# Performance work log

Hardware: AMD Instinct MI355X
Metric: run time of the kernel (lower is better)

Reference implementation:

```python
import jax, jax.numpy as jnp
import numpy as np

RATIO = 0.2
MIX_ALPHA = 0.5
TEMPERATURE = 0.1
EPS = 1e-12  # F.normalize eps


def setup_inputs() -> dict:
    key = jax.random.key(0)
    z = jax.random.normal(key, (16384, 256), dtype=jnp.float32)
    return {"z": z}


def reference(z):
    B = z.shape[0]
    n_hard = max(1, int(B * RATIO))

    # L2-normalize rows (F.normalize with eps clamp)
    norm = jnp.maximum(jnp.linalg.norm(z, axis=-1, keepdims=True), EPS)
    z_norm = z / norm

    # [B, B] cosine similarity, diagonal excluded
    sim = z_norm @ z_norm.T
    diag = jnp.eye(B, dtype=bool)
    sim = jnp.where(diag, -jnp.inf, sim)
    logits = sim / TEMPERATURE  # softmax(logits) == sim_probs

    # Batched sampling: replaces the per-sample Python loop with one fused pass
    key = jax.random.key(42)
    k_src, k_tgt, k_alpha = jax.random.split(key, 3)
    src_idx = jax.random.randint(k_src, (n_hard,), 0, B)  # torch.randint
    # categorical over logits rows == multinomial over softmax probs
    tgt_idx = jax.random.categorical(k_tgt, logits[src_idx], axis=-1)
    alpha = jax.random.uniform(k_alpha, (n_hard, 1), dtype=z.dtype) * MIX_ALPHA

    hard_negs = alpha * z[src_idx] + (1.0 - alpha) * z[tgt_idx]  # [n_hard, D]
    return hard_negs
```

## Files before the change

### kernel.cpp

```cpp
#include <hip/hip_runtime.h>
#include <stdint.h>
#include <math.h>

#define BN 16384
#define DK 256
#define NH 3276
#define NJB 52
#define NCB 128
#define NTILE (NJB * NCB)

typedef __attribute__((ext_vector_type(8))) short short8;
typedef __attribute__((ext_vector_type(4))) short short4v;
typedef __attribute__((ext_vector_type(4))) float f32x4;

__host__ __device__ __forceinline__ void tf2x32(uint32_t k0, uint32_t k1,
                                                uint32_t c0, uint32_t c1,
                                                uint32_t& o0, uint32_t& o1) {
  uint32_t ks2 = 0x1BD11BDAu ^ k0 ^ k1;
  uint32_t x0 = c0 + k0, x1 = c1 + k1;
#define RR(d) { x0 += x1; x1 = (x1 << d) | (x1 >> (32 - d)); x1 ^= x0; }
  RR(13) RR(15) RR(26) RR(6)   x0 += k1;  x1 += ks2 + 1u;
  RR(17) RR(29) RR(16) RR(24)  x0 += ks2; x1 += k0  + 2u;
  RR(13) RR(15) RR(26) RR(6)   x0 += k0;  x1 += k1  + 3u;
  RR(17) RR(29) RR(16) RR(24)  x0 += k1;  x1 += ks2 + 4u;
  RR(13) RR(15) RR(26) RR(6)   x0 += ks2; x1 += k0  + 5u;
#undef RR
  o0 = x0; o1 = x1;
}

__device__ __forceinline__ uint32_t rand32_at(uint32_t k0, uint32_t k1, uint32_t p) {
  uint32_t x0, x1; tf2x32(k0, k1, 0u, p, x0, x1);
  return x0 ^ x1;
}

__device__ __forceinline__ float unif01_from_bits(uint32_t bits) {
  return __uint_as_float((bits >> 9) | 0x3f800000u) - 1.0f;
}

__device__ __forceinline__ float gumbel_at(uint32_t k0, uint32_t k1, uint32_t p) {
  uint32_t bits = rand32_at(k0, k1, p);
  float f = unif01_from_bits(bits);
  float u = fmaxf(f, 1.17549435e-38f);
  float t = __log2f(u) * (-0.69314718055994531f);
  return __log2f(t) * (-0.69314718055994531f);
}

__device__ __forceinline__ unsigned long long packvc(float v, uint32_t c) {
  uint32_t u = __float_as_uint(v);
  u ^= ((int32_t)u < 0) ? 0xFFFFFFFFu : 0x80000000u;
  return ((unsigned long long)u << 32) | (unsigned long long)(~c);
}

__device__ __forceinline__ void glds16(const unsigned short* g, short* l) {
  __builtin_amdgcn_global_load_lds(
      (const __attribute__((address_space(1))) void*)g,
      (__attribute__((address_space(3))) void*)l, 16, 0, 0);
}

__global__ __launch_bounds__(256) void k_prep(const float* __restrict__ z,
                                              unsigned short* __restrict__ zh,
                                              unsigned short* __restrict__ zl,
                                              int* __restrict__ src_idx,
                                              unsigned long long* __restrict__ best,
                                              uint32_t k20, uint32_t k21) {
  int b = blockIdx.x, t = threadIdx.x;
  if (b < BN / 4) {
    int row = b * 4 + (t >> 6), lane = t & 63;
    float4 v = *(const float4*)&z[row * DK + lane * 4];
    float ss = v.x * v.x + v.y * v.y + v.z * v.z + v.w * v.w;
#pragma unroll
    for (int off = 32; off; off >>= 1) ss += __shfl_xor(ss, off, 64);
    float inv = 1.0f / fmaxf(sqrtf(ss), 1e-12f);
    float f[4] = {v.x * inv, v.y * inv, v.z * inv, v.w * inv};
    short4v h, l;
#pragma unroll
    for (int i = 0; i < 4; ++i) {
      uint32_t u = __float_as_uint(f[i]);
      h[i] = (short)(u >> 16);
      float r = f[i] - __uint_as_float(u & 0xFFFF0000u);
      l[i] = (short)(__float_as_uint(r) >> 16);
    }
    *(short4v*)&zh[row * DK + lane * 4] = h;
    *(short4v*)&zl[row * DK + lane * 4] = l;
  } else {
    int i = (b - BN / 4) * 256 + t;
    if (i < NH) {
      uint32_t bits = rand32_at(k20, k21, (uint32_t)i);
      src_idx[i] = (int)(bits & (uint32_t)(BN - 1));
      best[i] = 0ull;
    }
  }
}

__global__ __launch_bounds__(256, 4) void k_main(const unsigned short* __restrict__ zh,
                                                 const unsigned short* __restrict__ zl,
                                                 const int* __restrict__ src_idx,
                                                 unsigned long long* __restrict__ best,
                                                 uint32_t kt0, uint32_t kt1) {
  __shared__ __align__(16) short As_hi[64 * 32];
  __shared__ __align__(16) short As_lo[64 * 32];
  __shared__ __align__(16) short Bs_hi[128 * 32];
  __shared__ __align__(16) short Bs_lo[128 * 32];

  const int flat = blockIdx.x;
  const int xcd = flat & 7, slot = flat >> 3;
  const int c_base = (xcd * 16 + (slot & 15)) * 128;
  const int j_base = (slot >> 4) * 64;

  const int t = threadIdx.x;
  const int lane = t & 63, w = t >> 6;

  const int ra = w * 16 + (lane >> 2);
  const int rb0 = w * 32 + (lane >> 2);
  const int rb1 = rb0 + 16;
  const int ua = (lane & 3) ^ ((ra >> 1) & 3);
  const int ub0 = (lane & 3) ^ ((rb0 >> 1) & 3);
  const int ub1 = (lane & 3) ^ ((rb1 >> 1) & 3);
  const uint32_t offA = (uint32_t)(src_idx[min(j_base + ra, NH - 1)] * DK + ua * 8);
  const uint32_t offB0 = (uint32_t)((c_base + rb0) * DK + ub0 * 8);
  const uint32_t offB1 = (uint32_t)((c_base + rb1) * DK + ub1 * 8);
  short* dA  = &As_hi[w * 512];
  short* dAl = &As_lo[w * 512];
  short* dB  = &Bs_hi[w * 1024];
  short* dBl = &Bs_lo[w * 1024];

  const int mh = w >> 1, ch = w & 1;
  const int cl = lane & 15, q = lane >> 4;
  int foffA[2], foffB[4];
#pragma unroll
  for (int i = 0; i < 2; ++i) {
    int r = mh * 32 + cl + i * 16;
    foffA[i] = r * 32 + (q ^ ((r >> 1) & 3)) * 8;
  }
#pragma unroll
  for (int i = 0; i < 4; ++i) {
    int r = ch * 64 + cl + i * 16;
    foffB[i] = r * 32 + (q ^ ((r >> 1) & 3)) * 8;
  }

  const int q4 = q * 4;
  const int coff = c_base + ch * 64;
  const int roff = j_base + mh * 32;
  const uint32_t ccl = (uint32_t)(coff + cl);

  f32x4 acc[2][4];
#pragma unroll
  for (int mt = 0; mt < 2; ++mt)
#pragma unroll
    for (int nt = 0; nt < 4; ++nt) acc[mt][nt] = (f32x4){0.f, 0.f, 0.f, 0.f};

  float gum[32];

  glds16(zh + offA, dA);
  glds16(zl + offA, dAl);
  glds16(zh + offB0, dB);
  glds16(zh + offB1, dB + 512);
  glds16(zl + offB0, dBl);
  glds16(zl + offB1, dBl + 512);

#pragma unroll
  for (int kc = 0; kc < 8; ++kc) {
    __syncthreads();

    short8 ah[2], al[2], bh[4], bl[4];
#pragma unroll
    for (int nt = 0; nt < 4; ++nt) {
      bh[nt] = *(const short8*)&Bs_hi[foffB[nt]];
      bl[nt] = *(const short8*)&Bs_lo[foffB[nt]];
    }
#pragma unroll
    for (int mt = 0; mt < 2; ++mt) {
      ah[mt] = *(const short8*)&As_hi[foffA[mt]];
      al[mt] = *(const short8*)&As_lo[foffA[mt]];
    }
    __syncthreads();

    if (kc < 7) {
      const int ko = (kc + 1) * 32;
      glds16(zh + offA + ko, dA);
      glds16(zl + offA + ko, dAl);
      glds16(zh + offB0 + ko, dB);
      glds16(zh + offB1 + ko, dB + 512);
      glds16(zl + offB0 + ko, dBl);
      glds16(zl + offB1 + ko, dBl + 512);
    }

#pragma unroll
    for (int mt = 0; mt < 2; ++mt)
#pragma unroll
      for (int nt = 0; nt < 4; ++nt) {
        acc[mt][nt] = __builtin_amdgcn_mfma_f32_16x16x32_bf16(ah[mt], bh[nt], acc[mt][nt], 0, 0, 0);
        acc[mt][nt] = __builtin_amdgcn_mfma_f32_16x16x32_bf16(ah[mt], bl[nt], acc[mt][nt], 0, 0, 0);
        acc[mt][nt] = __builtin_amdgcn_mfma_f32_16x16x32_bf16(al[mt], bh[nt], acc[mt][nt], 0, 0, 0);
      }

#pragma unroll
    for (int i = 0; i < 4; ++i) {
      const int idx = kc * 4 + i;
      const int mt = idx >> 4, r = (idx >> 2) & 3, nt = idx & 3;
      int gj = roff + mt * 16 + q4 + r;
      uint32_t p = (uint32_t)gj * (uint32_t)BN + ccl + (uint32_t)(nt * 16);
      float gv = gumbel_at(kt0, kt1, p);
      asm volatile("" : "+v"(gv));
      gum[idx] = gv;
    }
  }

#pragma unroll
  for (int mt = 0; mt < 2; ++mt)
#pragma unroll
    for (int r = 0; r < 4; ++r) {
      int gj = roff + mt * 16 + q4 + r;
      int s = src_idx[min(gj, NH - 1)];
      float bv = -INFINITY; uint32_t bc = 0;
#pragma unroll
      for (int nt = 0; nt < 4; ++nt) {
        uint32_t c = ccl + (uint32_t)(nt * 16);
        float tot = fmaf(acc[mt][nt][r], 10.0f, gum[((mt * 4 + r) * 4) + nt]);
        tot = ((int)c == s) ? -INFINITY : tot;
        if (tot > bv) { bv = tot; bc = c; }
      }
      unsigned long long key = packvc(bv, bc);
#pragma unroll
      for (int off = 1; off <= 8; off <<= 1) {
        unsigned long long o = __shfl_xor(key, off, 64);
        if (o > key) key = o;
      }
      if (cl == 0 && gj < NH) atomicMax(&best[gj], key);
    }
}

__global__ __launch_bounds__(64) void k_out(const float* __restrict__ z,
                                            const int* __restrict__ src_idx,
                                            const unsigned long long* __restrict__ best,
                                            float* __restrict__ out,
                                            uint32_t ka0, uint32_t ka1) {
  int j = blockIdx.x;
  int lane = threadIdx.x;
  int s = src_idx[j];
  int tgt = (int)(~((uint32_t)(best[j] & 0xFFFFFFFFull)));
  uint32_t bits = rand32_at(ka0, ka1, (uint32_t)j);
  float alpha = unif01_from_bits(bits) * 0.5f;
  float om = 1.0f - alpha;
  float4 a = *(const float4*)&z[s * DK + lane * 4];
  float4 b = *(const float4*)&z[tgt * DK + lane * 4];
  float4 o;
  o.x = alpha * a.x + om * b.x;
  o.y = alpha * a.y + om * b.y;
  o.z = alpha * a.z + om * b.z;
  o.w = alpha * a.w + om * b.w;
  *(float4*)&out[j * DK + lane * 4] = o;
}

extern "C" void kernel_launch(void* const* d_in, const int* in_sizes, int n_in,
                              void* d_out, int out_size, void* d_ws, size_t ws_size,
                              hipStream_t stream) {
  const float* z = (const float*)d_in[0];
  float* out = (float*)d_out;
  char* ws = (char*)d_ws;
  int*                src_idx = (int*)(ws);
  unsigned long long* best    = (unsigned long long*)(ws + 16384);
  unsigned short*     zh      = (unsigned short*)(ws + 65536);
  unsigned short*     zl      = (unsigned short*)(ws + 65536 + 8388608);

  uint32_t r0 = 0u, r1 = 42u;
  uint32_t ks0, ks1, kt0, kt1, ka0, ka1, k20, k21;
  tf2x32(r0, r1, 0u, 0u, ks0, ks1);
  tf2x32(r0, r1, 0u, 1u, kt0, kt1);
  tf2x32(r0, r1, 0u, 2u, ka0, ka1);
  tf2x32(ks0, ks1, 0u, 1u, k20, k21);

  k_prep<<<dim3(BN / 4 + (NH + 255) / 256), dim3(256), 0, stream>>>(
      z, zh, zl, src_idx, best, k20, k21);
  k_main<<<dim3(NTILE), dim3(256), 0, stream>>>(zh, zl, src_idx, best, kt0, kt1);
  k_out <<<dim3(NH), dim3(64), 0, stream>>>(z, src_idx, best, out, ka0, ka1);
}
```

Measured before the change: 245.7 us.

## Make main kernel persistent over row tiles and pack output rows per block

Launches 1024 blocks for the main kernel instead of 6656. Each block keeps its column block and loops over 6–7 row tiles with a stride of 8, prefetching the next tile's A and B during the last k-chunk. This is meant to reduce block launch and tail overhead, although the B tile is still reloaded from global memory on every row tile. The output kernel now handles four rows per 256-thread block, cutting the number of blocks.

```diff
diff --git a/kernel.cpp b/kernel.cpp
--- a/kernel.cpp
+++ b/kernel.cpp
@@ -6,8 +6,7 @@
 #define DK 256
 #define NH 3276
 #define NJB 52
-#define NCB 128
-#define NTILE (NJB * NCB)
+#define NBLK 1024
 
 typedef __attribute__((ext_vector_type(8))) short short8;
 typedef __attribute__((ext_vector_type(4))) short short4v;
@@ -102,10 +101,12 @@
   __shared__ __align__(16) short Bs_hi[128 * 32];
   __shared__ __align__(16) short Bs_lo[128 * 32];
 
-  const int flat = blockIdx.x;
-  const int xcd = flat & 7, slot = flat >> 3;
-  const int c_base = (xcd * 16 + (slot & 15)) * 128;
-  const int j_base = (slot >> 4) * 64;
+  const int b = blockIdx.x;
+  const int xcd = b & 7;
+  const int cslot = (b >> 3) & 15;
+  const int c_base = (xcd * 16 + cslot) * 128;
+  const int j0 = b >> 7;
+  const int ntiles = (j0 < 4) ? 7 : 6;
 
   const int t = threadIdx.x;
   const int lane = t & 63, w = t >> 6;
@@ -116,7 +117,6 @@
   const int ua = (lane & 3) ^ ((ra >> 1) & 3);
   const int ub0 = (lane & 3) ^ ((rb0 >> 1) & 3);
   const int ub1 = (lane & 3) ^ ((rb1 >> 1) & 3);
-  const uint32_t offA = (uint32_t)(src_idx[min(j_base + ra, NH - 1)] * DK + ua * 8);
   const uint32_t offB0 = (uint32_t)((c_base + rb0) * DK + ub0 * 8);
   const uint32_t offB1 = (uint32_t)((c_base + rb1) * DK + ub1 * 8);
   short* dA  = &As_hi[w * 512];
@@ -140,17 +140,9 @@
 
   const int q4 = q * 4;
   const int coff = c_base + ch * 64;
-  const int roff = j_base + mh * 32;
   const uint32_t ccl = (uint32_t)(coff + cl);
 
-  f32x4 acc[2][4];
-#pragma unroll
-  for (int mt = 0; mt < 2; ++mt)
-#pragma unroll
-    for (int nt = 0; nt < 4; ++nt) acc[mt][nt] = (f32x4){0.f, 0.f, 0.f, 0.f};
-
-  float gum[32];
-
+  uint32_t offA = (uint32_t)(src_idx[min(j0 * 64 + ra, NH - 1)] * DK + ua * 8);
   glds16(zh + offA, dA);
   glds16(zl + offA, dAl);
   glds16(zh + offB0, dB);
@@ -158,85 +150,111 @@
   glds16(zl + offB0, dBl);
   glds16(zl + offB1, dBl + 512);
 
-#pragma unroll
-  for (int kc = 0; kc < 8; ++kc) {
-    __syncthreads();
-
-    short8 ah[2], al[2], bh[4], bl[4];
-#pragma unroll
-    for (int nt = 0; nt < 4; ++nt) {
-      bh[nt] = *(const short8*)&Bs_hi[foffB[nt]];
-      bl[nt] = *(const short8*)&Bs_lo[foffB[nt]];
+  for (int it = 0; it < ntiles; ++it) {
+    const int j_base = (j0 + 8 * it) * 64;
+    const int roff = j_base + mh * 32;
+    const bool have_next = (it + 1 < ntiles);
+    uint32_t nextA = 0;
+    if (have_next)
+      nextA = (uint32_t)(src_idx[min((j0 + 8 * (it + 1)) * 64 + ra, NH - 1)] * DK + ua * 8);
+
+    f32x4 acc[2][4];
+#pragma unroll
+    for (int mt = 0; mt < 2; ++mt)
+#pragma unroll
+      for (int nt = 0; nt < 4; ++nt) acc[mt][nt] = (f32x4){0.f, 0.f, 0.f, 0.f};
+
+    float gum[32];
+
+#pragma unroll
+    for (int kc = 0; kc < 8; ++kc) {
+      __syncthreads();
+
+      short8 ah[2], al[2], bh[4], bl[4];
+#pragma unroll
+      for (int nt = 0; nt < 4; ++nt) {
+        bh[nt] = *(const short8*)&Bs_hi[foffB[nt]];
+        bl[nt] = *(const short8*)&Bs_lo[foffB[nt]];
+      }
+#pragma unroll
+      for (int mt = 0; mt < 2; ++mt) {
+        ah[mt] = *(const short8*)&As_hi[foffA[mt]];
+        al[mt] = *(const short8*)&As_lo[foffA[mt]];
+      }
+      __syncthreads();
+
+      if (kc < 7) {
+        const int ko = (kc + 1) * 32;
+        glds16(zh + offA + ko, dA);
+        glds16(zl + offA + ko, dAl);
+        glds16(zh + offB0 + ko, dB);
+        glds16(zh + offB1 + ko, dB + 512);
+        glds16(zl + offB0 + ko, dBl);
+        glds16(zl + offB1 + ko, dBl + 512);
+      } else if (have_next) {
+        glds16(zh + nextA, dA);
+        glds16(zl + nextA, dAl);
+        glds16(zh + offB0, dB);
+        glds16(zh + offB1, dB + 512);
+        glds16(zl + offB0, dBl);
+        glds16(zl + offB1, dBl + 512);
+      }
+
+#pragma unroll
+      for (int mt = 0; mt < 2; ++mt)
+#pragma unroll
+        for (int nt = 0; nt < 4; ++nt) {
+          acc[mt][nt] = __builtin_amdgcn_mfma_f32_16x16x32_bf16(ah[mt], bh[nt], acc[mt][nt], 0, 0, 0);
+          acc[mt][nt] = __builtin_amdgcn_mfma_f32_16x16x32_bf16(ah[mt], bl[nt], acc[mt][nt], 0, 0, 0);
+          acc[mt][nt] = __builtin_amdgcn_mfma_f32_16x16x32_bf16(al[mt], bh[nt], acc[mt][nt], 0, 0, 0);
+        }
+
+#pragma unroll
+      for (int i = 0; i < 4; ++i) {
+        const int idx = kc * 4 + i;
+        const int mt = idx >> 4, r = (idx >> 2) & 3, nt = idx & 3;
+        int gj = roff + mt * 16 + q4 + r;
+        uint32_t p = (uint32_t)gj * (uint32_t)BN + ccl + (uint32_t)(nt * 16);
+        float gv = gumbel_at(kt0, kt1, p);
+        asm volatile("" : "+v"(gv));
+        gum[idx] = gv;
+      }
     }
-#pragma unroll
-    for (int mt = 0; mt < 2; ++mt) {
-      ah[mt] = *(const short8*)&As_hi[foffA[mt]];
-      al[mt] = *(const short8*)&As_lo[foffA[mt]];
-    }
-    __syncthreads();
-
-    if (kc < 7) {
-      const int ko = (kc + 1) * 32;
-      glds16(zh + offA + ko, dA);
-      glds16(zl + offA + ko, dAl);
-      glds16(zh + offB0 + ko, dB);
-      glds16(zh + offB1 + ko, dB + 512);
-      glds16(zl + offB0 + ko, dBl);
-      glds16(zl + offB1 + ko, dBl + 512);
-    }
+    offA = nextA;
 
 #pragma unroll
     for (int mt = 0; mt < 2; ++mt)
 #pragma unroll
-      for (int nt = 0; nt < 4; ++nt) {
-        acc[mt][nt] = __builtin_amdgcn_mfma_f32_16x16x32_bf16(ah[mt], bh[nt], acc[mt][nt], 0, 0, 0);
-        acc[mt][nt] = __builtin_amdgcn_mfma_f32_16x16x32_bf16(ah[mt], bl[nt], acc[mt][nt], 0, 0, 0);
-        acc[mt][nt] = __builtin_amdgcn_mfma_f32_16x16x32_bf16(al[mt], bh[nt], acc[mt][nt], 0, 0, 0);
-      }
-
-#pragma unroll
-    for (int i = 0; i < 4; ++i) {
-      const int idx = kc * 4 + i;
-      const int mt = idx >> 4, r = (idx >> 2) & 3, nt = idx & 3;
-      int gj = roff + mt * 16 + q4 + r;
-      uint32_t p = (uint32_t)gj * (uint32_t)BN + ccl + (uint32_t)(nt * 16);
-      float gv = gumbel_at(kt0, kt1, p);
-      asm volatile("" : "+v"(gv));
-      gum[idx] = gv;
-    }
-  }
-
-#pragma unroll
-  for (int mt = 0; mt < 2; ++mt)
-#pragma unroll
-    for (int r = 0; r < 4; ++r) {
-      int gj = roff + mt * 16 + q4 + r;
-      int s = src_idx[min(gj, NH - 1)];
-      float bv = -INFINITY; uint32_t bc = 0;
-#pragma unroll
-      for (int nt = 0; nt < 4; ++nt) {
-        uint32_t c = ccl + (uint32_t)(nt * 16);
-        float tot = fmaf(acc[mt][nt][r], 10.0f, gum[((mt * 4 + r) * 4) + nt]);
-        tot = ((int)c == s) ? -INFINITY : tot;
-        if (tot > bv) { bv = tot; bc = c; }
-      }
-      unsigned long long key = packvc(bv, bc);
-#pragma unroll
-      for (int off = 1; off <= 8; off <<= 1) {
-        unsigned long long o = __shfl_xor(key, off, 64);
-        if (o > key) key = o;
-      }
-      if (cl == 0 && gj < NH) atomicMax(&best[gj], key);
-    }
-}
-
-__global__ __launch_bounds__(64) void k_out(const float* __restrict__ z,
-                                            const int* __restrict__ src_idx,
-                                            const unsigned long long* __restrict__ best,
-                                            float* __restrict__ out,
-                                            uint32_t ka0, uint32_t ka1) {
-  int j = blockIdx.x;
-  int lane = threadIdx.x;
+      for (int r = 0; r < 4; ++r) {
+        int gj = roff + mt * 16 + q4 + r;
+        int s = src_idx[min(gj, NH - 1)];
+        float bv = -INFINITY; uint32_t bc = 0;
+#pragma unroll
+        for (int nt = 0; nt < 4; ++nt) {
+          uint32_t c = ccl + (uint32_t)(nt * 16);
+          float tot = fmaf(acc[mt][nt][r], 10.0f, gum[((mt * 4 + r) * 4) + nt]);
+          tot = ((int)c == s) ? -INFINITY : tot;
+          if (tot > bv) { bv = tot; bc = c; }
+        }
+        unsigned long long key = packvc(bv, bc);
+#pragma unroll
+        for (int off = 1; off <= 8; off <<= 1) {
+          unsigned long long o = __shfl_xor(key, off, 64);
+          if (o > key) key = o;
+        }
+        if (cl == 0 && gj < NH) atomicMax(&best[gj], key);
+      }
+  }
+}
+
+__global__ __launch_bounds__(256) void k_out(const float* __restrict__ z,
+                                             const int* __restrict__ src_idx,
+                                             const unsigned long long* __restrict__ best,
+                                             float* __restrict__ out,
+                                             uint32_t ka0, uint32_t ka1) {
+  int j = blockIdx.x * 4 + (threadIdx.x >> 6);
+  if (j >= NH) return;
+  int lane = threadIdx.x & 63;
   int s = src_idx[j];
   int tgt = (int)(~((uint32_t)(best[j] & 0xFFFFFFFFull)));
   uint32_t bits = rand32_at(ka0, ka1, (uint32_t)j);
@@ -272,6 +290,6 @@
 
   k_prep<<<dim3(BN / 4 + (NH + 255) / 256), dim3(256), 0, stream>>>(
       z, zh, zl, src_idx, best, k20, k21);
-  k_main<<<dim3(NTILE), dim3(256), 0, stream>>>(zh, zl, src_idx, best, kt0, kt1);
-  k_out <<<dim3(NH), dim3(64), 0, stream>>>(z, src_idx, best, out, ka0, ka1);
-}
+  k_main<<<dim3(NBLK), dim3(256), 0, stream>>>(zh, zl, src_idx, best, kt0, kt1);
+  k_out <<<dim3((NH + 3) / 4), dim3(256), 0, stream>>>(z, src_idx, best, out, ka0, ka1);
+}
```

New measurement: 317.2 us. 1.29x slower.
